# Optimization experiments

Hardware: AMD Instinct MI355X
Metric: run time of the kernel (lower is better)

## Reference

```python
import jax, jax.numpy as jnp
import numpy as np

NUM_HEADS = 16
WINDOW = 128
PERSIST = 16


def setup_inputs() -> dict:
    key = jax.random.key(0)
    ks = jax.random.split(key, 6)
    B, S, D, L = 2, 2048, 2048, 512
    sd = 1.0 / np.sqrt(D)
    sl = 1.0 / np.sqrt(L)
    return {
        "x": jax.random.normal(ks[0], (B, S, D), dtype=jnp.float32),
        "Wq": jax.random.normal(ks[1], (D, D), dtype=jnp.float32) * sd,
        "Wkv": jax.random.normal(ks[2], (D, L), dtype=jnp.float32) * sd,
        "Wk": jax.random.normal(ks[3], (L, D), dtype=jnp.float32) * sl,
        "Wv": jax.random.normal(ks[4], (L, D), dtype=jnp.float32) * sl,
        "Wo": jax.random.normal(ks[5], (D, D), dtype=jnp.float32) * sd,
    }


def reference(x, Wq, Wkv, Wk, Wv, Wo):
    B, S, D = x.shape
    H = NUM_HEADS
    hd = D // H
    scale = hd ** -0.5

    q = (x @ Wq).reshape(B, S, H, hd)
    kv_latent = x @ Wkv                      # MLA-style latent bottleneck
    k = (kv_latent @ Wk).reshape(B, S, H, hd)
    v = (kv_latent @ Wv).reshape(B, S, H, hd)

    # causal + sliding-window + persistent attention-sink mask
    qi = jnp.arange(S)[:, None]
    ki = jnp.arange(S)[None, :]
    mask = (ki <= qi) & ((qi - ki < WINDOW) | (ki < PERSIST))  # [S,S]

    scores = jnp.einsum("bqhd,bkhd->bhqk", q, k) * scale
    scores = jnp.where(mask[None, None], scores, jnp.finfo(scores.dtype).min)
    attn = jax.nn.softmax(scores, axis=-1)
    out = jnp.einsum("bhqk,bkhd->bqhd", attn, v).reshape(B, S, D)
    return out @ Wo
```

## Files before the change

### kernel.cpp

```cpp
#include <hip/hip_runtime.h>

typedef float f32x4 __attribute__((ext_vector_type(4)));
typedef float f32x16 __attribute__((ext_vector_type(16)));
typedef __bf16 bf16x8 __attribute__((ext_vector_type(8)));

__device__ __forceinline__ short f2bf(float f) {
    union { float f; unsigned u; } x; x.f = f;
    unsigned r = x.u + 0x7fffu + ((x.u >> 16) & 1u);
    return (short)(r >> 16);
}

__device__ __forceinline__ void store_out(float* p, float v) { *p = v; }
__device__ __forceinline__ void store_out(short* p, float v) { *p = f2bf(v); }

__device__ __forceinline__ void gload_lds16(const short* g, short* l) {
    __builtin_amdgcn_global_load_lds(
        (__attribute__((address_space(1))) void*)(void*)g,
        (__attribute__((address_space(3))) void*)l, 16, 0, 0);
}

__global__ void prep_all(const float* __restrict__ x, short* __restrict__ xb,
                         const float* __restrict__ Wq, const float* __restrict__ Wo,
                         const float* __restrict__ Wk, const float* __restrict__ Wv,
                         const float* __restrict__ Wkv,
                         short* __restrict__ WqkvT, short* __restrict__ WoT,
                         short* __restrict__ WkT, short* __restrict__ WvT) {
    __shared__ float tile[32][33];
    int id = blockIdx.x;
    const int t = threadIdx.x;
    if (id < 8192) {
        const int i = id * 256 + t;
        float4 v = ((const float4*)x)[i];
        ((short4*)xb)[i] = make_short4(f2bf(v.x), f2bf(v.y), f2bf(v.z), f2bf(v.w));
        return;
    }
    id -= 8192;
    const float* in; short* out; int R, C, xt, yt;
    if (id < 4096)       { in = Wq;  out = WqkvT; R = 2048; C = 2048; xt = id & 63; yt = id >> 6; }
    else if (id < 8192)  { id -= 4096; in = Wo;  out = WoT;  R = 2048; C = 2048; xt = id & 63; yt = id >> 6; }
    else if (id < 9216)  { id -= 8192; in = Wk;  out = WkT;  R = 512;  C = 2048; xt = id & 63; yt = id >> 6; }
    else if (id < 10240) { id -= 9216; in = Wv;  out = WvT;  R = 512;  C = 2048; xt = id & 63; yt = id >> 6; }
    else                 { id -= 10240; in = Wkv; out = WqkvT + (size_t)2048 * 2048;
                           R = 2048; C = 512; xt = id & 15; yt = id >> 4; }
    const int c0 = xt * 32, r0 = yt * 32;
    const int tx = t & 31, ty = t >> 5;
#pragma unroll
    for (int i = 0; i < 32; i += 8)
        tile[ty + i][tx] = in[(size_t)(r0 + ty + i) * C + c0 + tx];
    __syncthreads();
#pragma unroll
    for (int i = 0; i < 32; i += 8)
        out[(size_t)(c0 + ty + i) * R + r0 + tx] = f2bf(tile[tx][ty + i]);
}

template <typename OutT>
__device__ __forceinline__ void gemm32_core(
    const short* __restrict__ A, const short* __restrict__ Bt, OutT* __restrict__ C,
    int m0, int n0, int K, int lda, int ldb, int ldc, short* sA, short* sB) {
    const int t = threadIdx.x;
    const int w = t >> 6, l = t & 63;
    const int wr = w >> 1, wc = w & 1;
    const int lrow = l & 31, lhalf = l >> 5;

    f32x16 acc[2][2] = {};

    const int r_off = w * 32 + (l >> 3);
    const int c8 = (((l & 7) ^ (l >> 3)) & 7) * 8;
    const short* aB = A + (size_t)(m0 + r_off) * lda + c8;
    const short* bB = Bt + (size_t)(n0 + r_off) * ldb + c8;
    short* sAw = sA + w * 2048;
    short* sBw = sB + w * 2048;

    for (int kk = 0; kk < K; kk += 64) {
#pragma unroll
        for (int p = 0; p < 4; ++p) {
            gload_lds16(aB + kk + (size_t)(p * 8) * lda, sAw + p * 512);
            gload_lds16(bB + kk + (size_t)(p * 8) * ldb, sBw + p * 512);
        }
        __syncthreads();
#pragma unroll
        for (int ks = 0; ks < 4; ++ks) {
            const int c = ks * 2 + lhalf;
            bf16x8 af[2], bfr[2];
#pragma unroll
            for (int mi = 0; mi < 2; ++mi) {
                const int m = wr * 64 + mi * 32 + lrow;
                af[mi] = *(const bf16x8*)&sA[m * 64 + (c ^ (m & 7)) * 8];
            }
#pragma unroll
            for (int ni = 0; ni < 2; ++ni) {
                const int n = wc * 64 + ni * 32 + lrow;
                bfr[ni] = *(const bf16x8*)&sB[n * 64 + (c ^ (n & 7)) * 8];
            }
#pragma unroll
            for (int mi = 0; mi < 2; ++mi)
#pragma unroll
                for (int ni = 0; ni < 2; ++ni)
                    acc[mi][ni] = __builtin_amdgcn_mfma_f32_32x32x16_bf16(
                        af[mi], bfr[ni], acc[mi][ni], 0, 0, 0);
        }
        __syncthreads();
    }
#pragma unroll
    for (int mi = 0; mi < 2; ++mi)
#pragma unroll
        for (int ni = 0; ni < 2; ++ni) {
            const int col = n0 + wc * 64 + ni * 32 + lrow;
#pragma unroll
            for (int r = 0; r < 16; ++r) {
                const int row = m0 + wr * 64 + mi * 32 + (r & 3) + 8 * (r >> 2) + 4 * lhalf;
                store_out(&C[(size_t)row * ldc + col], acc[mi][ni][r]);
            }
        }
}

template <typename OutT>
__global__ __launch_bounds__(256, 2)
void gemm32(const short* __restrict__ A, const short* __restrict__ Bt,
            OutT* __restrict__ C, int K, int lda, int ldb, int ldc) {
    __shared__ __align__(16) short sA[128 * 64];
    __shared__ __align__(16) short sB[128 * 64];
    gemm32_core<OutT>(A, Bt, C, blockIdx.y * 128, blockIdx.x * 128, K, lda, ldb, ldc, sA, sB);
}

#define LBASE(buf, kh, ab) ((((((buf) << 1) | (kh)) << 1) | (ab)) * 8192)

#define STAGE(P, ld, tt, kh, buf, ab)                                   \
    do {                                                                \
        const int kb_ = (tt) * 64 + (kh) * 32;                          \
        const short* s_ = (P) + kb_;                                    \
        short* d_ = lds + LBASE(buf, kh, ab) + w * 512;                 \
        gload_lds16(s_, d_);                                            \
        gload_lds16(s_ + (size_t)128 * (ld), d_ + 4096);                \
    } while (0)

#define VM6 asm volatile("s_waitcnt vmcnt(6)" ::: "memory")

#define MFMA16(a, b, c) __builtin_amdgcn_mfma_f32_16x16x32_bf16(a, b, c, 0, 0, 0)

#define MM_ROW(mi, areg)                                                \
    acc[mi][0] = MFMA16(areg, bv0, acc[mi][0]);                         \
    acc[mi][1] = MFMA16(areg, bv1, acc[mi][1]);                         \
    acc[mi][2] = MFMA16(areg, bv2, acc[mi][2]);                         \
    acc[mi][3] = MFMA16(areg, bv3, acc[mi][3]);

#define HALFK(buf, kh, STG0, W0, STG1)                                  \
    {                                                                   \
        bf16x8 bv0, bv1, bv2, bv3;                                      \
        {                                                               \
            const short* Ab_ = lds + LBASE(buf, kh, 0) + (wm * 128) * 32 + foff; \
            const short* Bb_ = lds + LBASE(buf, kh, 1) + (wn * 64) * 32 + foff;  \
            bf16x8 a0_ = *(const bf16x8*)&Ab_[0];                       \
            bf16x8 a1_ = *(const bf16x8*)&Ab_[512];                     \
            bf16x8 a2_ = *(const bf16x8*)&Ab_[1024];                    \
            bf16x8 a3_ = *(const bf16x8*)&Ab_[1536];                    \
            bv0 = *(const bf16x8*)&Bb_[0];                              \
            bv1 = *(const bf16x8*)&Bb_[512];                            \
            bv2 = *(const bf16x8*)&Bb_[1024];                           \
            bv3 = *(const bf16x8*)&Bb_[1536];                           \
            STG0;                                                       \
            W0;                                                         \
            __builtin_amdgcn_s_barrier();                               \
            asm volatile("s_waitcnt lgkmcnt(0)" ::: "memory");          \
            __builtin_amdgcn_sched_barrier(0);                          \
            __builtin_amdgcn_s_setprio(1);                              \
            MM_ROW(0, a0_) MM_ROW(1, a1_) MM_ROW(2, a2_) MM_ROW(3, a3_) \
            __builtin_amdgcn_s_setprio(0);                              \
            __builtin_amdgcn_s_barrier();                               \
        }                                                               \
        {                                                               \
            const short* Ab_ = lds + LBASE(buf, kh, 0) + (wm * 128 + 64) * 32 + foff; \
            bf16x8 a0_ = *(const bf16x8*)&Ab_[0];                       \
            bf16x8 a1_ = *(const bf16x8*)&Ab_[512];                     \
            bf16x8 a2_ = *(const bf16x8*)&Ab_[1024];                    \
            bf16x8 a3_ = *(const bf16x8*)&Ab_[1536];                    \
            STG1;                                                       \
            __builtin_amdgcn_s_barrier();                               \
            asm volatile("s_waitcnt lgkmcnt(0)" ::: "memory");          \
            __builtin_amdgcn_sched_barrier(0);                          \
            __builtin_amdgcn_s_setprio(1);                              \
            MM_ROW(4, a0_) MM_ROW(5, a1_) MM_ROW(6, a2_) MM_ROW(7, a3_) \
            __builtin_amdgcn_s_setprio(0);                              \
            __builtin_amdgcn_s_barrier();                               \
        }                                                               \
    }

template <typename OutT>
__device__ __forceinline__ void gemm256_core(
    const short* __restrict__ A, const short* __restrict__ Bt, OutT* __restrict__ C,
    int m0, int n0, int K, int lda, int ldb, int ldc, short* lds) {
    const int t = threadIdx.x;
    const int w = t >> 6, l = t & 63;
    const int wm = w >> 2, wn = w & 3;
    const int l15 = l & 15, lc = l >> 4;

    const int su = (l & 7) ^ ((l >> 3) & 7);
    const int srow = (w << 4) + ((l >> 3) << 1) + (su >> 2);
    const int scol = (su & 3) << 3;
    const short* Ag = A + (size_t)(m0 + srow) * lda + scol;
    const short* Bg = Bt + (size_t)(n0 + srow) * ldb + scol;

    const int i3 = ((((l15 & 1) << 2) | lc) ^ ((l15 >> 1) & 7));
    const int foff = (l15 >> 1) * 64 + i3 * 8;

    f32x4 acc[8][4] = {};

    const int ntm1 = (K >> 6) - 1;
    const int niter = K >> 7;

    STAGE(Ag, lda, 0, 0, 0, 0);
    STAGE(Bg, ldb, 0, 0, 0, 1);
    STAGE(Ag, lda, 0, 1, 0, 0);
    STAGE(Bg, ldb, 0, 1, 0, 1);
    STAGE(Ag, lda, 1, 0, 1, 0);
    STAGE(Bg, ldb, 1, 0, 1, 1);
    asm volatile("s_waitcnt vmcnt(8)" ::: "memory");
    __builtin_amdgcn_s_barrier();

#pragma unroll 1
    for (int it = 0; it < niter; ++it) {
        const int tt = it * 2;
        const int t1 = tt + 1;
        const int t2 = (tt + 2 > ntm1) ? ntm1 : tt + 2;
        const int t3 = (tt + 3 > ntm1) ? ntm1 : tt + 3;
        HALFK(0, 0, STAGE(Ag, lda, t1, 1, 1, 0), VM6, STAGE(Bg, ldb, t1, 1, 1, 1))
        HALFK(0, 1, STAGE(Ag, lda, t2, 0, 0, 0), VM6, STAGE(Bg, ldb, t2, 0, 0, 1))
        HALFK(1, 0, STAGE(Ag, lda, t2, 1, 0, 0), VM6, STAGE(Bg, ldb, t2, 1, 0, 1))
        HALFK(1, 1, STAGE(Ag, lda, t3, 0, 1, 0), VM6, STAGE(Bg, ldb, t3, 0, 1, 1))
    }

    asm volatile("s_waitcnt vmcnt(0)" ::: "memory");

    const int crow = m0 + wm * 128 + lc * 4;
    const int ccol = n0 + wn * 64 + l15;
#pragma unroll
    for (int mi = 0; mi < 8; ++mi)
#pragma unroll
        for (int ni = 0; ni < 4; ++ni) {
            OutT* cp = C + (size_t)(crow + mi * 16) * ldc + ccol + ni * 16;
#pragma unroll
            for (int rr = 0; rr < 4; ++rr)
                store_out(cp + (size_t)rr * ldc, acc[mi][ni][rr]);
        }
}

__global__ __launch_bounds__(512, 2)
void gemm256_kv(const short* __restrict__ kvl, const short* __restrict__ WkT,
                short* __restrict__ kk, const short* __restrict__ WvT,
                short* __restrict__ vT) {
    extern __shared__ short lds[];
    int id = blockIdx.x;
    if (id < 128) {
        gemm256_core<short>(kvl, WkT, kk, (id >> 3) * 256, (id & 7) * 256,
                            512, 2560, 512, 2048, lds);
    } else {
        id -= 128;
        gemm256_core<short>(WvT, kvl, vT, (id >> 4) * 256, (id & 15) * 256,
                            512, 512, 2560, 4096, lds);
    }
}

#define A_S 2048
#define A_D 2048
#define A_M 4096
#define A_HD 128
__global__ __launch_bounds__(256)
void attn_win3(const short* __restrict__ Q, const short* __restrict__ K,
               const short* __restrict__ vT, short* __restrict__ O, int ldq) {
    const int qt = blockIdx.x, h = blockIdx.y, b = blockIdx.z;
    const int Qs = qt * 64;
    const int t = threadIdx.x, w = t >> 6, l = t & 63;
    const int qs = Qs + w * 16;
    const int lg = l >> 4, ln = l & 15;
    const float SCALE = 0.088388347648318447f;

    __shared__ __align__(16) short sK[2][512 * 8];
    __shared__ __align__(16) short sV[2][512 * 8];
    __shared__ __align__(16) short sP[4][16][40];

    const size_t bS = (size_t)b * A_S;
    const short* qrow = Q + (bS + qs + ln) * ldq + h * A_HD;
    bf16x8 qf[4];
#pragma unroll
    for (int ks = 0; ks < 4; ++ks)
        qf[ks] = *(const bf16x8*)(qrow + ks * 32 + lg * 8);

    f32x4 o[8] = {};
    float lsum[4] = {0.f, 0.f, 0.f, 0.f};

    int C_lo = (Qs - 127) >> 5; if (C_lo < 0) C_lo = 0;
    const int C_hi = (Qs + 63) >> 5;
    const bool sink = C_lo > 0;
    const int total = (C_hi - C_lo + 1) + (sink ? 1 : 0);

    const int key0 = t >> 4, dseg0s = (t & 15) ^ (key0 & 7);
    const int d0 = t >> 2, ksg0 = (t & 3) ^ ((d0 >> 1) & 3);
    const int key1 = (256 + t) >> 4, dseg1s = (t & 15) ^ (key1 & 7);
    const int d1 = (256 + t) >> 2, ksg1 = (t & 3) ^ ((d1 >> 1) & 3);
    const short* Kb = K + bS * A_D + h * A_HD;
    const short* Vb = vT + (size_t)h * A_HD * A_M + b * A_S;

#define ASTAGE(kb, buf)                                                         \
    do {                                                                        \
        gload_lds16(Kb + (size_t)((kb) + key0) * A_D + dseg0s * 8,              \
                    &sK[buf][(size_t)(w * 64) * 8]);                            \
        gload_lds16(Vb + (size_t)d0 * A_M + (kb) + ksg0 * 8,                    \
                    &sV[buf][(size_t)(w * 64) * 8]);                            \
        gload_lds16(Kb + (size_t)((kb) + key1) * A_D + dseg1s * 8,              \
                    &sK[buf][(size_t)(256 + w * 64) * 8]);                      \
        gload_lds16(Vb + (size_t)d1 * A_M + (kb) + ksg1 * 8,                    \
                    &sV[buf][(size_t)(256 + w * 64) * 8]);                      \
    } while (0)

#define CHUNK_KB(ci) ((((sink) && (ci) == 0) ? 0 : (C_lo + (ci) - (sink ? 1 : 0))) * 32)

    ASTAGE(CHUNK_KB(0), 0);
    __syncthreads();

    for (int ci = 0; ci < total; ++ci) {
        if (ci + 1 < total) {
            const int nkb = CHUNK_KB(ci + 1);
            ASTAGE(nkb, (ci + 1) & 1);
        }
        const int kb = CHUNK_KB(ci);
        const int buf = ci & 1;
        const bool any = (kb < 16) || ((kb + 31 >= qs - 127) && (kb <= qs + 15));
        if (any) {
            f32x4 s0 = {0.f, 0.f, 0.f, 0.f}, s1 = {0.f, 0.f, 0.f, 0.f};
#pragma unroll
            for (int ks = 0; ks < 4; ++ks) {
                const int dsg = ks * 4 + lg;
                bf16x8 k0 = *(const bf16x8*)&sK[buf][(ln * 16 + (dsg ^ (ln & 7))) * 8];
                bf16x8 k1 = *(const bf16x8*)&sK[buf][((16 + ln) * 16 + (dsg ^ (ln & 7))) * 8];
                s0 = __builtin_amdgcn_mfma_f32_16x16x32_bf16(qf[ks], k0, s0, 0, 0, 0);
                s1 = __builtin_amdgcn_mfma_f32_16x16x32_bf16(qf[ks], k1, s1, 0, 0, 0);
            }
            const int k0i = kb + ln, k1i = kb + 16 + ln;
#pragma unroll
            for (int r = 0; r < 4; ++r) {
                const int qi = qs + lg * 4 + r;
                const bool m0 = (k0i <= qi) && ((qi - k0i < 128) || (k0i < 16));
                const bool m1 = (k1i <= qi) && ((qi - k1i < 128) || (k1i < 16));
                const float p0 = m0 ? __expf(s0[r] * SCALE) : 0.f;
                const float p1 = m1 ? __expf(s1[r] * SCALE) : 0.f;
                lsum[r] += p0 + p1;
                sP[w][lg * 4 + r][ln] = f2bf(p0);
                sP[w][lg * 4 + r][16 + ln] = f2bf(p1);
            }
            bf16x8 pf = *(const bf16x8*)&sP[w][ln][lg * 8];
#pragma unroll
            for (int dgi = 0; dgi < 8; ++dgi) {
                const int d = dgi * 16 + ln;
                bf16x8 vf = *(const bf16x8*)&sV[buf][(d * 4 + (lg ^ ((ln >> 1) & 3))) * 8];
                o[dgi] = __builtin_amdgcn_mfma_f32_16x16x32_bf16(pf, vf, o[dgi], 0, 0, 0);
            }
        }
        __syncthreads();
    }
#undef ASTAGE
#undef CHUNK_KB

#pragma unroll
    for (int r = 0; r < 4; ++r) {
        float s = lsum[r];
        s += __shfl_xor(s, 1); s += __shfl_xor(s, 2);
        s += __shfl_xor(s, 4); s += __shfl_xor(s, 8);
        const float inv = 1.0f / s;
        short* orow = O + (bS + qs + lg * 4 + r) * A_D + h * A_HD + ln;
#pragma unroll
        for (int dgi = 0; dgi < 8; ++dgi)
            orow[dgi * 16] = f2bf(o[dgi][r] * inv);
    }
}

extern "C" void kernel_launch(void* const* d_in, const int* in_sizes, int n_in,
                              void* d_out, int out_size, void* d_ws, size_t ws_size,
                              hipStream_t stream) {
    (void)in_sizes; (void)n_in; (void)out_size; (void)ws_size;
    const float* x   = (const float*)d_in[0];
    const float* Wq  = (const float*)d_in[1];
    const float* Wkv = (const float*)d_in[2];
    const float* Wk  = (const float*)d_in[3];
    const float* Wv  = (const float*)d_in[4];
    const float* Wo  = (const float*)d_in[5];
    float* out = (float*)d_out;

    const int B = 2, S = 2048, D = 2048, L = 512, H = 16;
    const int M = B * S;
    const int NQ = D + L;

    short* p = (short*)d_ws;
    short* xb    = p; p += (size_t)M * D;
    short* WqkvT = p; p += (size_t)NQ * D;
    short* WkT   = p; p += (size_t)D * L;
    short* WvT   = p; p += (size_t)D * L;
    short* WoT   = p; p += (size_t)D * D;
    short* qkv   = p; p += (size_t)M * NQ;
    short* kk    = p; p += (size_t)M * D;
    short* vT    = p; p += (size_t)D * M;
    short* ao    = p; p += (size_t)M * D;

    static bool attr_done = false;
    if (!attr_done) {
        hipFuncSetAttribute((const void*)&gemm256_kv,
                            hipFuncAttributeMaxDynamicSharedMemorySize, 131072);
        attr_done = true;
    }

    prep_all<<<19456, 256, 0, stream>>>(x, xb, Wq, Wo, Wk, Wv, Wkv,
                                        WqkvT, WoT, WkT, WvT);
    gemm32<short><<<dim3(NQ / 128, M / 128), 256, 0, stream>>>(
        xb, WqkvT, qkv, D, D, D, NQ);
    gemm256_kv<<<256, 512, 131072, stream>>>(qkv + D, WkT, kk, WvT, vT);

    attn_win3<<<dim3(S / 64, H, B), 256, 0, stream>>>(qkv, kk, vT, ao, NQ);

    gemm32<float><<<dim3(D / 128, M / 128), 256, 0, stream>>>(
        ao, WoT, out, D, D, D, D);
}
```

Baseline: 269.3 us.

## Overlap weight transposes with QKV GEMM and add pipelined output GEMM

```diff
diff --git a/kernel.cpp b/kernel.cpp
--- a/kernel.cpp
+++ b/kernel.cpp
@@ -20,11 +20,8 @@
 }
 
 __global__ void prep_all(const float* __restrict__ x, short* __restrict__ xb,
-                         const float* __restrict__ Wq, const float* __restrict__ Wo,
-                         const float* __restrict__ Wk, const float* __restrict__ Wv,
-                         const float* __restrict__ Wkv,
-                         short* __restrict__ WqkvT, short* __restrict__ WoT,
-                         short* __restrict__ WkT, short* __restrict__ WvT) {
+                         const float* __restrict__ Wq, const float* __restrict__ Wkv,
+                         short* __restrict__ WqkvT) {
     __shared__ float tile[32][33];
     int id = blockIdx.x;
     const int t = threadIdx.x;
@@ -36,12 +33,9 @@
     }
     id -= 8192;
     const float* in; short* out; int R, C, xt, yt;
-    if (id < 4096)       { in = Wq;  out = WqkvT; R = 2048; C = 2048; xt = id & 63; yt = id >> 6; }
-    else if (id < 8192)  { id -= 4096; in = Wo;  out = WoT;  R = 2048; C = 2048; xt = id & 63; yt = id >> 6; }
-    else if (id < 9216)  { id -= 8192; in = Wk;  out = WkT;  R = 512;  C = 2048; xt = id & 63; yt = id >> 6; }
-    else if (id < 10240) { id -= 9216; in = Wv;  out = WvT;  R = 512;  C = 2048; xt = id & 63; yt = id >> 6; }
-    else                 { id -= 10240; in = Wkv; out = WqkvT + (size_t)2048 * 2048;
-                           R = 2048; C = 512; xt = id & 15; yt = id >> 4; }
+    if (id < 4096) { in = Wq;  out = WqkvT; R = 2048; C = 2048; xt = id & 63; yt = id >> 6; }
+    else           { id -= 4096; in = Wkv; out = WqkvT + (size_t)2048 * 2048;
+                     R = 2048; C = 512; xt = id & 15; yt = id >> 4; }
     const int c0 = xt * 32, r0 = yt * 32;
     const int tx = t & 31, ty = t >> 5;
 #pragma unroll
@@ -114,13 +108,37 @@
         }
 }
 
-template <typename OutT>
 __global__ __launch_bounds__(256, 2)
-void gemm32(const short* __restrict__ A, const short* __restrict__ Bt,
-            OutT* __restrict__ C, int K, int lda, int ldb, int ldc) {
+void gemm32qkv(const short* __restrict__ A, const short* __restrict__ Bt,
+               short* __restrict__ C,
+               const float* __restrict__ Wo, const float* __restrict__ Wk,
+               const float* __restrict__ Wv,
+               short* __restrict__ WoT, short* __restrict__ WkT,
+               short* __restrict__ WvT) {
     __shared__ __align__(16) short sA[128 * 64];
     __shared__ __align__(16) short sB[128 * 64];
-    gemm32_core<OutT>(A, Bt, C, blockIdx.y * 128, blockIdx.x * 128, K, lda, ldb, ldc, sA, sB);
+    int id = blockIdx.x;
+    if (id < 640) {
+        gemm32_core<short>(A, Bt, C, (id / 20) * 128, (id % 20) * 128,
+                           2048, 2048, 2048, 2560, sA, sB);
+        return;
+    }
+    id -= 640;
+    float (*tile)[33] = (float(*)[33])sA;
+    const float* in; short* out; int R, Cc, xt, yt;
+    if (id < 4096)      { in = Wo; out = WoT; R = 2048; Cc = 2048; xt = id & 63; yt = id >> 6; }
+    else if (id < 5120) { id -= 4096; in = Wk; out = WkT; R = 512; Cc = 2048; xt = id & 63; yt = id >> 6; }
+    else                { id -= 5120; in = Wv; out = WvT; R = 512; Cc = 2048; xt = id & 63; yt = id >> 6; }
+    const int c0 = xt * 32, r0 = yt * 32;
+    const int t = threadIdx.x;
+    const int tx = t & 31, ty = t >> 5;
+#pragma unroll
+    for (int i = 0; i < 32; i += 8)
+        tile[ty + i][tx] = in[(size_t)(r0 + ty + i) * Cc + c0 + tx];
+    __syncthreads();
+#pragma unroll
+    for (int i = 0; i < 32; i += 8)
+        out[(size_t)(c0 + ty + i) * R + r0 + tx] = f2bf(tile[tx][ty + i]);
 }
 
 #define LBASE(buf, kh, ab) ((((((buf) << 1) | (kh)) << 1) | (ab)) * 8192)
@@ -260,6 +278,103 @@
     }
 }
 
+#define LB2(s) ((s) * 12288)
+
+#define STG2(ps, pt)                                                    \
+    do {                                                                \
+        const int kb_ = (pt) * 32;                                      \
+        gload_lds16(Ag + kb_, lds + LB2(ps) + w * 512);                 \
+        gload_lds16(Ag + kb_ + (size_t)128 * lda, lds + LB2(ps) + 4096 + w * 512); \
+        gload_lds16(Bg + kb_, lds + LB2(ps) + 8192 + w * 512);          \
+    } while (0)
+
+#define PH2(s, ps, pt)                                                  \
+    {                                                                   \
+        const short* Ab_ = lds + LB2(s) + wm * 2048 + foff;             \
+        const short* Bb_ = lds + LB2(s) + 8192 + wn * 2048 + foff;      \
+        bf16x8 a0_ = *(const bf16x8*)&Ab_[0];                           \
+        bf16x8 a1_ = *(const bf16x8*)&Ab_[512];                         \
+        bf16x8 a2_ = *(const bf16x8*)&Ab_[1024];                        \
+        bf16x8 a3_ = *(const bf16x8*)&Ab_[1536];                        \
+        bf16x8 b0_ = *(const bf16x8*)&Bb_[0];                           \
+        bf16x8 b1_ = *(const bf16x8*)&Bb_[512];                         \
+        bf16x8 b2_ = *(const bf16x8*)&Bb_[1024];                        \
+        bf16x8 b3_ = *(const bf16x8*)&Bb_[1536];                        \
+        STG2(ps, pt);                                                   \
+        asm volatile("s_waitcnt vmcnt(6)" ::: "memory");                \
+        __builtin_amdgcn_s_barrier();                                   \
+        asm volatile("s_waitcnt lgkmcnt(0)" ::: "memory");              \
+        __builtin_amdgcn_sched_barrier(0);                              \
+        __builtin_amdgcn_s_setprio(1);                                  \
+        acc[0][0]=MFMA16(a0_,b0_,acc[0][0]); acc[0][1]=MFMA16(a0_,b1_,acc[0][1]); \
+        acc[0][2]=MFMA16(a0_,b2_,acc[0][2]); acc[0][3]=MFMA16(a0_,b3_,acc[0][3]); \
+        acc[1][0]=MFMA16(a1_,b0_,acc[1][0]); acc[1][1]=MFMA16(a1_,b1_,acc[1][1]); \
+        acc[1][2]=MFMA16(a1_,b2_,acc[1][2]); acc[1][3]=MFMA16(a1_,b3_,acc[1][3]); \
+        acc[2][0]=MFMA16(a2_,b0_,acc[2][0]); acc[2][1]=MFMA16(a2_,b1_,acc[2][1]); \
+        acc[2][2]=MFMA16(a2_,b2_,acc[2][2]); acc[2][3]=MFMA16(a2_,b3_,acc[2][3]); \
+        acc[3][0]=MFMA16(a3_,b0_,acc[3][0]); acc[3][1]=MFMA16(a3_,b1_,acc[3][1]); \
+        acc[3][2]=MFMA16(a3_,b2_,acc[3][2]); acc[3][3]=MFMA16(a3_,b3_,acc[3][3]); \
+        __builtin_amdgcn_s_setprio(0);                                  \
+        __builtin_amdgcn_s_barrier();                                   \
+    }
+
+__global__ __launch_bounds__(512, 2)
+void gemm_out(const short* __restrict__ A, const short* __restrict__ Bt,
+              float* __restrict__ C, int K, int lda, int ldb, int ldc) {
+    extern __shared__ short lds[];
+    const int m0 = blockIdx.y * 256, n0 = blockIdx.x * 128;
+    const int t = threadIdx.x;
+    const int w = t >> 6, l = t & 63;
+    const int wm = w >> 1, wn = w & 1;
+    const int l15 = l & 15, lc = l >> 4;
+
+    const int su = (l & 7) ^ ((l >> 3) & 7);
+    const int srow = (w << 4) + ((l >> 3) << 1) + (su >> 2);
+    const int scol = (su & 3) << 3;
+    const short* Ag = A + (size_t)(m0 + srow) * lda + scol;
+    const short* Bg = Bt + (size_t)(n0 + srow) * ldb + scol;
+
+    const int i3 = ((((l15 & 1) << 2) | lc) ^ ((l15 >> 1) & 7));
+    const int foff = (l15 >> 1) * 64 + i3 * 8;
+
+    f32x4 acc[4][4] = {};
+
+    const int nkh1 = (K >> 5) - 1;
+
+    STG2(0, 0);
+    STG2(1, 1);
+    STG2(2, 2);
+    asm volatile("s_waitcnt vmcnt(6)" ::: "memory");
+    __builtin_amdgcn_s_barrier();
+
+#pragma unroll 1
+    for (int it = 0; it < (K >> 7); ++it) {
+        const int h0 = it * 4;
+        const int p3 = h0 + 3;
+        const int p4 = (h0 + 4 > nkh1) ? nkh1 : h0 + 4;
+        const int p5 = (h0 + 5 > nkh1) ? nkh1 : h0 + 5;
+        const int p6 = (h0 + 6 > nkh1) ? nkh1 : h0 + 6;
+        PH2(0, 3, p3)
+        PH2(1, 0, p4)
+        PH2(2, 1, p5)
+        PH2(3, 2, p6)
+    }
+
+    asm volatile("s_waitcnt vmcnt(0)" ::: "memory");
+
+    const int crow = m0 + wm * 64 + lc * 4;
+    const int ccol = n0 + wn * 64 + l15;
+#pragma unroll
+    for (int mi = 0; mi < 4; ++mi)
+#pragma unroll
+        for (int ni = 0; ni < 4; ++ni) {
+            float* cp = C + (size_t)(crow + mi * 16) * ldc + ccol + ni * 16;
+#pragma unroll
+            for (int rr = 0; rr < 4; ++rr)
+                store_out(cp + (size_t)rr * ldc, acc[mi][ni][rr]);
+        }
+}
+
 #define A_S 2048
 #define A_D 2048
 #define A_M 4096
@@ -404,17 +519,18 @@
     if (!attr_done) {
         hipFuncSetAttribute((const void*)&gemm256_kv,
                             hipFuncAttributeMaxDynamicSharedMemorySize, 131072);
+        hipFuncSetAttribute((const void*)&gemm_out,
+                            hipFuncAttributeMaxDynamicSharedMemorySize, 98304);
         attr_done = true;
     }
 
-    prep_all<<<19456, 256, 0, stream>>>(x, xb, Wq, Wo, Wk, Wv, Wkv,
-                                        WqkvT, WoT, WkT, WvT);
-    gemm32<short><<<dim3(NQ / 128, M / 128), 256, 0, stream>>>(
-        xb, WqkvT, qkv, D, D, D, NQ);
+    prep_all<<<13312, 256, 0, stream>>>(x, xb, Wq, Wkv, WqkvT);
+    gemm32qkv<<<6784, 256, 0, stream>>>(xb, WqkvT, qkv, Wo, Wk, Wv,
+                                        WoT, WkT, WvT);
     gemm256_kv<<<256, 512, 131072, stream>>>(qkv + D, WkT, kk, WvT, vT);
 
     attn_win3<<<dim3(S / 64, H, B), 256, 0, stream>>>(qkv, kk, vT, ao, NQ);
 
-    gemm32<float><<<dim3(D / 128, M / 128), 256, 0, stream>>>(
+    gemm_out<<<dim3(D / 128, M / 256), 512, 98304, stream>>>(
         ao, WoT, out, D, D, D, D);
 }
```

After: 260.6 us. -3.3%, faster.
